# Optimization experiments

Hardware: AMD Instinct MI355X
Metric: run time of the kernel (lower is better)

The kernel has to match this reference:

```python
import jax, jax.numpy as jnp
import numpy as np

B, N, F_IN, F_OUT, K = 128, 400, 128, 128, 5


def setup_inputs() -> dict:
    key = jax.random.key(0)
    ks = jax.random.split(key, 7)
    s_in = 1.0 / np.sqrt(F_IN)
    s_out = 1.0 / np.sqrt(F_OUT)
    return {
        "x": jax.random.normal(ks[0], (B, N, F_IN), dtype=jnp.float32),
        # SAGEConv layer 1: lin_l (neighbor agg, with bias) and lin_r (root, no bias)
        "W1l": jax.random.normal(ks[1], (F_OUT, F_IN), dtype=jnp.float32) * s_in,
        "b1l": jnp.zeros((F_OUT,), dtype=jnp.float32),
        "W1r": jax.random.normal(ks[2], (F_OUT, F_IN), dtype=jnp.float32) * s_in,
        # SAGEConv layer 2
        "W2l": jax.random.normal(ks[3], (F_OUT, F_OUT), dtype=jnp.float32) * s_out,
        "b2l": jnp.zeros((F_OUT,), dtype=jnp.float32),
        "W2r": jax.random.normal(ks[4], (F_OUT, F_OUT), dtype=jnp.float32) * s_out,
    }


def _knn_sym_adj(x):
    # x: [B, N, F]. Per-batch 5-NN graph with self-loops (loop=True),
    # then symmetrized (to_undirected coalesces duplicates -> 0/1 adjacency).
    sq = jnp.sum(x * x, axis=-1)                       # [B, N]
    d2 = sq[:, :, None] + sq[:, None, :] - 2.0 * jnp.einsum("bnd,bmd->bnm", x, x)
    _, idx = jax.lax.top_k(-d2, K)                     # [B, N, K] nearest incl. self
    A = jnp.zeros((x.shape[0], x.shape[1], x.shape[1]), dtype=x.dtype)
    bi = jnp.arange(x.shape[0])[:, None, None]
    ni = jnp.arange(x.shape[1])[None, :, None]
    A = A.at[bi, ni, idx].set(1.0)                     # A[b,i,j]=1 if j in knn(i)
    return jnp.maximum(A, A.transpose(0, 2, 1))        # undirected


def _sage(h, A, deg, Wl, bl, Wr):
    # PyG SAGEConv (mean aggr): out = lin_l(mean_j x_j) + lin_r(x_i)
    m = jnp.einsum("bnm,bmf->bnf", A, h) / deg
    return m @ Wl.T + bl + h @ Wr.T


def reference(x, W1l, b1l, W1r, W2l, b2l, W2r):
    A = _knn_sym_adj(x)
    deg = jnp.sum(A, axis=-1, keepdims=True)           # >=1 (self-loop)
    h = jax.nn.relu(_sage(x, A, deg, W1l, b1l, W1r))
    h = _sage(h, A, deg, W2l, b2l, W2r)
    return h.reshape(B * N, F_OUT)
```

## Files before the change

kernel.cpp:

```cpp
#include <hip/hip_runtime.h>
#include <hip/hip_bf16.h>
#include <stdint.h>

#define B_   128
#define N_   400
#define F_   128
#define K_   5
#define ROWS (B_ * N_)
#define POOLCAP 2048
#define DCAP 416
#define MAXFLAG ROWS
#define GAP_HEDGE 5e-4
#define DELTA_MAX 0.18f
#define NW 13

typedef __attribute__((ext_vector_type(8))) short bf16x8;
typedef __attribute__((ext_vector_type(4))) float f32x4;

static __device__ __forceinline__ unsigned short f2bf(float f) {
  union { float f; unsigned u; } v; v.f = f;
  unsigned r = v.u + 0x7fff + ((v.u >> 16) & 1);
  return (unsigned short)(r >> 16);
}
static __device__ __forceinline__ float bf2f(unsigned short h) {
  union { unsigned u; float f; } v; v.u = ((unsigned)h) << 16; return v.f;
}

template<int M, typename T>
static __device__ __forceinline__ void insM(T d, int j, T bd[], int bj[]) {
  if (d < bd[M - 1] || (d == bd[M - 1] && j < bj[M - 1])) {
    bd[M - 1] = d; bj[M - 1] = j;
#pragma unroll
    for (int q = M - 1; q > 0; --q) {
      bool sw = (bd[q] < bd[q - 1]) || (bd[q] == bd[q - 1] && bj[q] < bj[q - 1]);
      T td = bd[q]; int tj = bj[q];
      if (sw) { bd[q] = bd[q - 1]; bd[q - 1] = td; bj[q] = bj[q - 1]; bj[q - 1] = tj; }
    }
  }
}

__global__ __launch_bounds__(256) void k_prep_rows(const float* __restrict__ x,
                                                   unsigned short* __restrict__ Y,
                                                   float* __restrict__ sq) {
  int wave = threadIdx.x >> 6, lane = threadIdx.x & 63;
  int row = blockIdx.x * 4 + wave;
  float2 v = *(const float2*)&x[(size_t)row * F_ + lane * 2];
  unsigned short hx = f2bf(v.x), hy = f2bf(v.y);
  float lx = v.x - bf2f(hx), ly = v.y - bf2f(hy);
  *(unsigned*)&Y[(size_t)row * 256 + lane * 2]       = (unsigned)hx | ((unsigned)hy << 16);
  *(unsigned*)&Y[(size_t)row * 256 + 128 + lane * 2] = (unsigned)f2bf(lx) | ((unsigned)f2bf(ly) << 16);
  float s = v.x * v.x + v.y * v.y;
#pragma unroll
  for (int o = 32; o > 0; o >>= 1) s += __shfl_xor(s, o);
  if (lane == 0) sq[row] = s;
}

__global__ __launch_bounds__(256) void k_prep_w(const float* __restrict__ W1l,
                                                const float* __restrict__ W1r,
                                                const float* __restrict__ W2l,
                                                const float* __restrict__ W2r,
                                                unsigned short* __restrict__ Wh,
                                                unsigned short* __restrict__ Wlo) {
  int t = blockIdx.x * 256 + threadIdx.x;
  int m = t >> 14, e = t & 16383;
  const float* src = (m == 0) ? W1l : (m == 1) ? W1r : (m == 2) ? W2l : W2r;
  float f = src[e];
  unsigned short h = f2bf(f);
  Wh[t] = h;
  Wlo[t] = f2bf(f - bf2f(h));
}

#define YJ_STRIDE 264
__global__ __launch_bounds__(256) void k_knn(const unsigned short* __restrict__ Y,
                                             const float* __restrict__ sq,
                                             int* __restrict__ idxout,
                                             int* __restrict__ flagcnt,
                                             int* __restrict__ flagrows,
                                             int* __restrict__ cand) {
  __shared__ unsigned short Yj[64 * YJ_STRIDE];
  __shared__ float sqj[64];

  int b = blockIdx.y, i0 = blockIdx.x * 64;
  int tid = threadIdx.x, wave = tid >> 6, lane = tid & 63;

  int i_local = wave * 16 + (lane & 15);
  int arow = b * N_ + min(i0 + i_local, N_ - 1);
  float sqi = sq[arow];

  const bf16x8* abase = (const bf16x8*)&Y[(size_t)arow * 256];
  bf16x8 af[8];
#pragma unroll
  for (int kc = 0; kc < 8; ++kc) af[kc] = abase[kc * 4 + (lane >> 4)];

  float bd[8] = {3.4e38f, 3.4e38f, 3.4e38f, 3.4e38f, 3.4e38f, 3.4e38f, 3.4e38f, 3.4e38f};
  int   bj[8] = {1 << 30, 1 << 30, 1 << 30, 1 << 30, 1 << 30, 1 << 30, 1 << 30, 1 << 30};

  const float4* srcb = (const float4*)(Y + (size_t)b * N_ * 256);

  for (int jt = 0; jt < 7; ++jt) {
    int j0 = jt * 64;
    float4* dst4 = (float4*)Yj;
#pragma unroll
    for (int q = 0; q < 8; ++q) {
      int l = tid + 256 * q;
      int r = l >> 5, cc = l & 31;
      int jr = min(j0 + r, N_ - 1);
      dst4[r * 33 + cc] = srcb[jr * 32 + cc];
    }
    if (tid < 64) sqj[tid] = sq[b * N_ + min(j0 + tid, N_ - 1)];
    __syncthreads();

#pragma unroll
    for (int ct = 0; ct < 4; ++ct) {
      f32x4 acc = {0.f, 0.f, 0.f, 0.f};
      int jfr = ct * 16 + (lane & 15);
      const bf16x8* bbase = (const bf16x8*)&Yj[jfr * YJ_STRIDE];
#pragma unroll
      for (int kc = 0; kc < 12; ++kc) {
        int bidx = (kc & 3) * 4 + ((kc >= 8) ? 16 : 0) + (lane >> 4);
        acc = __builtin_amdgcn_mfma_f32_16x16x32_bf16(bbase[bidx], af[kc & 7], acc, 0, 0, 0);
      }
      int jbase = ct * 16 + (lane >> 4) * 4;
      float4 sjv = *(const float4*)&sqj[jbase];
      float sj4[4] = {sjv.x, sjv.y, sjv.z, sjv.w};
#pragma unroll
      for (int r = 0; r < 4; ++r) {
        int j = j0 + jbase + r;
        float d = sqi + sj4[r] - 2.0f * acc[r];
        if (j < N_) insM<8, float>(d, j, bd, bj);
      }
    }
    __syncthreads();
  }

  float* mbd = (float*)Yj;
  int*   mbj = (int*)Yj + 2048;
  int slot = i_local * 32 + (lane >> 4) * 8;
#pragma unroll
  for (int q = 0; q < 8; ++q) { mbd[slot + q] = bd[q]; mbj[slot + q] = bj[q]; }
  __syncthreads();

  if (tid < 64) {
    int i = i0 + tid;
    if (i < N_) {
      float fd[6] = {3.4e38f, 3.4e38f, 3.4e38f, 3.4e38f, 3.4e38f, 3.4e38f};
      int   fj[6] = {1 << 30, 1 << 30, 1 << 30, 1 << 30, 1 << 30, 1 << 30};
      for (int q = 0; q < 32; ++q)
        insM<6, float>(mbd[tid * 32 + q], mbj[tid * 32 + q], fd, fj);
      int gi = b * N_ + i;
#pragma unroll
      for (int q = 0; q < 5; ++q) idxout[gi * K_ + q] = fj[q];
      if (fd[5] - fd[4] < 0.02f) {
        int pos = atomicAdd(flagcnt, 1);
        if (pos < MAXFLAG) {
          flagrows[pos] = gi;
          for (int q = 0; q < 32; ++q) cand[gi * 32 + q] = mbj[tid * 32 + q];
        }
      }
    }
  }
}

__global__ __launch_bounds__(256) void k_refine(const float* __restrict__ x,
                                                const int* __restrict__ flagrows,
                                                const int* __restrict__ flagcnt,
                                                const int* __restrict__ cand,
                                                int* __restrict__ idx,
                                                int* __restrict__ hcnt,
                                                int* __restrict__ hrows,
                                                int* __restrict__ hab) {
  __shared__ double dbuf[8][32];
  __shared__ int    jbuf[8][32];
  int slot = threadIdx.x >> 5, c = threadIdx.x & 31;
  int nflag = min(*flagcnt, MAXFLAG);
  for (int base = blockIdx.x * 8; base < nflag; base += gridDim.x * 8) {
    int t = base + slot;
    __syncthreads();
    if (t < nflag) {
      int row = flagrows[t];
      int b = row / N_;
      int j = cand[row * 32 + c];
      const float* xi = x + (size_t)row * F_;
      const float* xj = x + (size_t)(b * N_ + j) * F_;
      double s = 0.0;
#pragma unroll
      for (int q = 0; q < 128; ++q) {
        double d = (double)xi[q] - (double)xj[q];
        s = fma(d, d, s);
      }
      dbuf[slot][c] = s; jbuf[slot][c] = j;
    }
    __syncthreads();
    if (c == 0 && t < nflag) {
      int row = flagrows[t];
      int b = row / N_;
      double fd[6] = {1e300, 1e300, 1e300, 1e300, 1e300, 1e300};
      int    fj[6] = {1 << 30, 1 << 30, 1 << 30, 1 << 30, 1 << 30, 1 << 30};
      for (int q = 0; q < 32; ++q) insM<6, double>(dbuf[slot][q], jbuf[slot][q], fd, fj);
#pragma unroll
      for (int q = 0; q < 5; ++q) idx[row * K_ + q] = fj[q];
      if (fd[5] - fd[4] < GAP_HEDGE) {
        int p = atomicAdd(hcnt, 1);
        if (p < MAXFLAG) {
          hrows[p] = row;
          hab[2 * p]     = b * N_ + fj[4];
          hab[2 * p + 1] = b * N_ + fj[5];
        }
      }
    }
  }
}

__global__ __launch_bounds__(512) void k_buildg(const int* __restrict__ idx,
                                                const int* __restrict__ c6,
                                                int* __restrict__ L6,
                                                float* __restrict__ W6,
                                                int* __restrict__ pooli,
                                                float* __restrict__ poolw,
                                                int* __restrict__ offi,
                                                int* __restrict__ cnti) {
  __shared__ unsigned bm1[N_][NW];
  __shared__ unsigned bmh[N_][NW];
  __shared__ int cs[512];
  int b = blockIdx.x, t = threadIdx.x;
  int gb0 = b * N_;

  for (int q = t; q < N_ * NW; q += 512) {
    (&bm1[0][0])[q] = 0u;
    (&bmh[0][0])[q] = 0u;
  }

  int i = t;
  int j0 = -1, j1 = -1, j2 = -1, j3 = -1, j4 = -1, y6 = -1;
  if (i < N_) {
    const int* ip = idx + (size_t)(gb0 + i) * 5;
    j0 = ip[0]; j1 = ip[1]; j2 = ip[2]; j3 = ip[3]; j4 = ip[4];
    y6 = c6[gb0 + i];
  }
  __syncthreads();

  if (i < N_) {
    unsigned bit = 1u << (i & 31);
    int w = i >> 5;
    if (j0 != i) atomicOr(&bm1[j0][w], bit);
    if (j1 != i) atomicOr(&bm1[j1][w], bit);
    if (j2 != i) atomicOr(&bm1[j2][w], bit);
    if (j3 != i) atomicOr(&bm1[j3][w], bit);
    if (j4 != i) {
      if (y6 >= 0) atomicOr(&bmh[j4][w], bit); else atomicOr(&bm1[j4][w], bit);
    }
    if (y6 >= 0 && y6 != i) atomicOr(&bmh[y6][w], bit);
  }
  __syncthreads();

  if (i < N_) {
    int gi = gb0 + i;
    int   jj[6]  = {j0, j1, j2, j3, j4, y6};
    float w1s[6] = {1.f, 1.f, 1.f, 1.f,
                    (y6 >= 0) ? 0.5f : 1.f,
                    (y6 >= 0) ? 0.5f : 0.f};
#pragma unroll
    for (int k = 0; k < 6; ++k) {
      int j = jj[k]; float w1 = w1s[k];
      size_t sl = (size_t)gi * 6 + k;
      if (w1 <= 0.f || j < 0) { L6[sl] = gi; W6[sl] = 0.f; continue; }
      if (j == i)             { L6[sl] = gi; W6[sl] = 1.f; continue; }
      float w2 = ((bm1[i][j >> 5] >> (j & 31)) & 1) ? 1.f
               : (((bmh[i][j >> 5] >> (j & 31)) & 1) ? 0.5f : 0.f);
      L6[sl] = gb0 + j; W6[sl] = fmaxf(w1, w2);
    }
  }

  unsigned mw[NW];
  int cnt_i = 0;
  if (i < N_) {
#pragma unroll
    for (int w = 0; w < NW; ++w) {
      unsigned ex = 0;
      if ((i  >> 5) == w) ex |= 1u << (i  & 31);
      if ((j0 >> 5) == w) ex |= 1u << (j0 & 31);
      if ((j1 >> 5) == w) ex |= 1u << (j1 & 31);
      if ((j2 >> 5) == w) ex |= 1u << (j2 & 31);
      if ((j3 >> 5) == w) ex |= 1u << (j3 & 31);
      if ((j4 >> 5) == w) ex |= 1u << (j4 & 31);
      if (y6 >= 0 && (y6 >> 5) == w) ex |= 1u << (y6 & 31);
      unsigned m = (bm1[i][w] | bmh[i][w]) & ~ex;
      mw[w] = m;
      cnt_i += __popc(m);
    }
  } else {
#pragma unroll
    for (int w = 0; w < NW; ++w) mw[w] = 0u;
  }

  cs[t] = (i < N_) ? cnt_i : 0;
  __syncthreads();
  for (int off = 1; off < 512; off <<= 1) {
    int v = (t >= off) ? cs[t - off] : 0;
    __syncthreads();
    cs[t] += v;
    __syncthreads();
  }

  if (i < N_) {
    int o = b * POOLCAP + cs[t] - cnt_i;
    offi[gb0 + i] = o;
    cnti[gb0 + i] = cnt_i;
    int c = 0;
#pragma unroll
    for (int w = 0; w < NW; ++w) {
      unsigned m = mw[w];
      unsigned ones = bm1[i][w];
      while (m) {
        int bit = __ffs(m) - 1; m &= m - 1;
        int r = w * 32 + bit;
        pooli[o + c] = gb0 + r;
        poolw[o + c] = ((ones >> bit) & 1) ? 1.f : 0.5f;
        ++c;
      }
    }
  }
}

__global__ __launch_bounds__(128) void k_delta(
    const float* __restrict__ P, const float* __restrict__ Qb,
    const float* __restrict__ b1, const unsigned short* __restrict__ h1b,
    const float* __restrict__ sumP, const float* __restrict__ degv,
    const int* __restrict__ L6, const float* __restrict__ W6,
    const int* __restrict__ pooli, const float* __restrict__ poolw,
    const int* __restrict__ offi, const int* __restrict__ cnti,
    const int* __restrict__ idx,
    const int* __restrict__ hcnt, const int* __restrict__ hrows,
    const int* __restrict__ hab,
    const float* __restrict__ W2l, const float* __restrict__ W2r,
    int* __restrict__ c6, float* __restrict__ w5) {
  __shared__ float H[3][2][128];
  __shared__ float dH[3][128];
  __shared__ float U[3][128];
  __shared__ float V1[128], V2[128], red[128];
  __shared__ int   Ls[3][DCAP];
  __shared__ float Wsh[3][DCAP];
  int f = threadIdx.x;
  int n = min(*hcnt, MAXFLAG);
  for (int t = blockIdx.x; t < n; t += gridDim.x) {
    int gi = hrows[t], ga = hab[2 * t], gb = hab[2 * t + 1];
    int bb = gi / N_, iw = gi - bb * N_;
    bool ma = false, mb = false;
#pragma unroll
    for (int q = 0; q < K_; ++q) {
      ma = ma || (idx[ga * K_ + q] == iw);
      mb = mb || (idx[gb * K_ + q] == iw);
    }
    if (ma && mb) continue;
    int rows3[3] = {gi, ga, gb};
    int nn3[3];
    for (int s3 = 0; s3 < 3; ++s3) {
      int r = rows3[s3];
      int cc = cnti[r], oo = offi[r];
      int nn = 6 + cc; nn3[s3] = nn;
      for (int e = f; e < DCAP; e += 128) {
        int li = -1; float lw = 0.f;
        if (e < 6)      { li = L6[(size_t)r * 6 + e]; lw = W6[(size_t)r * 6 + e]; }
        else if (e < nn){ li = pooli[oo + e - 6];     lw = poolw[oo + e - 6]; }
        Ls[s3][e] = li; Wsh[s3][e] = lw;
      }
    }
    for (int s3 = 0; s3 < 3; ++s3) {
      int r = rows3[s3];
      float s1 = sumP[(size_t)r * 128 + f], d1 = degv[r];
      float ds = 0.f, dd = 0.f;
      if (s3 == 0) {
        if (!ma) { ds -= P[(size_t)ga * 128 + f]; dd -= 1.f; }
        if (!mb) { ds += P[(size_t)gb * 128 + f]; dd += 1.f; }
      } else if (s3 == 1) {
        if (!ma) { ds -= P[(size_t)gi * 128 + f]; dd -= 1.f; }
      } else {
        if (!mb) { ds += P[(size_t)gi * 128 + f]; dd += 1.f; }
      }
      float base = b1[f] + Qb[(size_t)r * 128 + f];
      float h0 = fmaxf(s1 / d1 + base, 0.f);
      float h1v = fmaxf((s1 + ds) / (d1 + dd) + base, 0.f);
      H[s3][0][f] = h0;
      H[s3][1][f] = h1v;
      dH[s3][f] = h1v - h0;
    }
    __syncthreads();
    {
      float u0 = 0.f, u1 = 0.f, u2 = 0.f;
      for (int f2 = 0; f2 < 128; ++f2) {
        float wv = W2l[f * 128 + f2];
        u0 += dH[0][f2] * wv;
        u1 += dH[1][f2] * wv;
        u2 += dH[2][f2] * wv;
      }
      U[0][f] = u0; U[1][f] = u1; U[2][f] = u2;
    }
    __syncthreads();
    float dmax = 0.f;
    for (int which = 0; which < 3; ++which) {
      float v1 = 0.f, v2 = 0.f;
      float d1r = degv[rows3[which]], d2r = d1r;
      int nnw = nn3[which];
      for (int e2 = 0; e2 < nnw; ++e2) {
        float w = Wsh[which][e2];
        if (w == 0.f) continue;
        int s = Ls[which][e2];
        float hv1, hv2;
        if (s == gi)      { hv1 = H[0][0][f]; hv2 = H[0][1][f]; }
        else if (s == ga) { hv1 = H[1][0][f]; hv2 = H[1][1][f]; }
        else if (s == gb) { hv1 = H[2][0][f]; hv2 = H[2][1][f]; }
        else {
          float hh = bf2f(h1b[(size_t)s * 256 + f]) + bf2f(h1b[(size_t)s * 256 + 128 + f]);
          hv1 = hh; hv2 = hh;
        }
        bool inG2 = true;
        if (which == 0 && s == ga && !ma) inG2 = false;
        if (which == 1 && s == gi && !ma) inG2 = false;
        v1 += w * hv1;
        if (inG2) v2 += w * hv2; else d2r -= w;
      }
      if (which == 0 && !mb) { v2 += H[2][1][f]; d2r += 1.f; }
      if (which == 2 && !mb) { v2 += H[0][1][f]; d2r += 1.f; }
      V1[f] = v1; V2[f] = v2;
      __syncthreads();
      float a1 = 0.f, a2 = 0.f, ow = 0.f;
      for (int f2 = 0; f2 < 128; ++f2) {
        float wl = W2l[f * 128 + f2];
        a1 += V1[f2] * wl;
        a2 += V2[f2] * wl;
        ow += dH[which][f2] * W2r[f * 128 + f2];
      }
      dmax = fmaxf(dmax, fabsf(a2 / d2r - a1 / d1r + ow));
      __syncthreads();
    }
    for (int li = 0; li < 3; ++li) {
      for (int e = f; e < nn3[li]; e += 128) {
        float w = Wsh[li][e];
        if (w == 0.f) continue;
        int r = Ls[li][e];
        if (r == gi || r == ga || r == gb) continue;
        bool dup = false;
        for (int lj = 0; lj < li && !dup; ++lj)
          for (int e2 = 0; e2 < nn3[lj]; ++e2)
            if (Ls[lj][e2] == r && Wsh[lj][e2] != 0.f) { dup = true; break; }
        if (dup) continue;
        float wi = 0.f, wa = 0.f, wb = 0.f;
        if (li == 0) wi = w; else if (li == 1) wa = w; else wb = w;
        for (int lj = li + 1; lj < 3; ++lj)
          for (int e2 = 0; e2 < nn3[lj]; ++e2)
            if (Ls[lj][e2] == r && Wsh[lj][e2] != 0.f) {
              if (lj == 1) wa = Wsh[lj][e2]; else wb = Wsh[lj][e2];
            }
        float lm = 0.f;
        for (int ff = 0; ff < 128; ++ff)
          lm = fmaxf(lm, fabsf(wi * U[0][ff] + wa * U[1][ff] + wb * U[2][ff]));
        dmax = fmaxf(dmax, lm / degv[r]);
      }
    }
    red[f] = dmax;
    __syncthreads();
    for (int o = 64; o > 0; o >>= 1) {
      if (f < o) red[f] = fmaxf(red[f], red[f + o]);
      __syncthreads();
    }
    if (f == 0 && red[0] < DELTA_MAX) { c6[gi] = gb - bb * N_; w5[gi] = 0.5f; }
    __syncthreads();
  }
}

#define WSTR 130
__global__ __launch_bounds__(256) void k_gemm(const unsigned short* __restrict__ A,
                                              const unsigned short* __restrict__ Whl,
                                              const unsigned short* __restrict__ Whr,
                                              const unsigned short* __restrict__ Wll,
                                              const unsigned short* __restrict__ Wlr,
                                              float* __restrict__ P, float* __restrict__ Q) {
  __shared__ unsigned short W[4 * 128 * WSTR];
  int tid = threadIdx.x, wave = tid >> 6, lane = tid & 63;
#pragma unroll
  for (int q = 0; q < 2; ++q) {
    int ridx = tid * 2 + q;
    int mat = ridx >> 7, n = ridx & 127;
    const unsigned short* src =
        ((mat == 0) ? Whl : (mat == 1) ? Whr : (mat == 2) ? Wll : Wlr) + n * 128;
    unsigned short* dst = &W[(size_t)ridx * WSTR];
#pragma unroll
    for (int p = 0; p < 16; ++p) *(bf16x8*)(dst + p * 8) = *(const bf16x8*)(src + p * 8);
  }
  __syncthreads();

  size_t row = (size_t)blockIdx.x * 64 + wave * 16 + (lane & 15);
  bf16x8 af[8];
#pragma unroll
  for (int s = 0; s < 2; ++s)
#pragma unroll
    for (int kc = 0; kc < 4; ++kc)
      af[s * 4 + kc] = *(const bf16x8*)&A[row * 256 + s * 128 + kc * 32 + (lane >> 4) * 8];

  size_t orow0 = (size_t)blockIdx.x * 64 + wave * 16 + (lane >> 4) * 4;
#pragma unroll
  for (int w = 0; w < 2; ++w) {
    float* O = w ? Q : P;
#pragma unroll
    for (int ct = 0; ct < 8; ++ct) {
      f32x4 acc = {0.f, 0.f, 0.f, 0.f};
      int n = ct * 16 + (lane & 15);
      const unsigned short* bh = &W[(size_t)(w * 128 + n) * WSTR];
      const unsigned short* bl = &W[(size_t)((2 + w) * 128 + n) * WSTR];
#pragma unroll
      for (int kc = 0; kc < 4; ++kc) {
        bf16x8 fh = *(const bf16x8*)(bh + kc * 32 + (lane >> 4) * 8);
        bf16x8 fl_ = *(const bf16x8*)(bl + kc * 32 + (lane >> 4) * 8);
        acc = __builtin_amdgcn_mfma_f32_16x16x32_bf16(af[kc], fh, acc, 0, 0, 0);
        acc = __builtin_amdgcn_mfma_f32_16x16x32_bf16(af[4 + kc], fh, acc, 0, 0, 0);
        acc = __builtin_amdgcn_mfma_f32_16x16x32_bf16(af[kc], fl_, acc, 0, 0, 0);
      }
#pragma unroll
      for (int r = 0; r < 4; ++r)
        O[(orow0 + r) * 128 + ct * 16 + (lane & 15)] = acc[r];
    }
  }
}

__global__ __launch_bounds__(256) void k_aggr(const float* __restrict__ P,
                                              const float* __restrict__ Q,
                                              const int* __restrict__ L6,
                                              const float* __restrict__ W6,
                                              const int* __restrict__ pooli,
                                              const float* __restrict__ poolw,
                                              const int* __restrict__ offi,
                                              const int* __restrict__ cnti,
                                              const float* __restrict__ bias,
                                              float* __restrict__ outf,
                                              unsigned short* __restrict__ outb,
                                              float* __restrict__ sumP,
                                              float* __restrict__ degv,
                                              int relu) {
  int r = blockIdx.x * 8 + (threadIdx.x >> 5);
  int l4 = threadIdx.x & 31;
  int m = cnti[r], o = offi[r];
  float4 acc = {0.f, 0.f, 0.f, 0.f};
  float deg = 0.f;
#pragma unroll
  for (int k = 0; k < 6; ++k) {
    float ww = W6[(size_t)r * 6 + k];
    float4 p4 = *(const float4*)&P[(size_t)L6[(size_t)r * 6 + k] * 128 + l4 * 4];
    acc.x += ww * p4.x; acc.y += ww * p4.y;
    acc.z += ww * p4.z; acc.w += ww * p4.w;
    deg += ww;
  }
  for (int q = 0; q < m; ++q) {
    float ww = poolw[o + q];
    float4 p4 = *(const float4*)&P[(size_t)pooli[o + q] * 128 + l4 * 4];
    acc.x += ww * p4.x; acc.y += ww * p4.y;
    acc.z += ww * p4.z; acc.w += ww * p4.w;
    deg += ww;
  }
  if (sumP) {
    *(float4*)&sumP[(size_t)r * 128 + l4 * 4] = acc;
    if (l4 == 0) degv[r] = deg;
  }
  float4 b4 = *(const float4*)&bias[l4 * 4];
  float4 q4 = *(const float4*)&Q[(size_t)r * 128 + l4 * 4];
  float4 v;
  v.x = acc.x / deg + b4.x + q4.x;
  v.y = acc.y / deg + b4.y + q4.y;
  v.z = acc.z / deg + b4.z + q4.z;
  v.w = acc.w / deg + b4.w + q4.w;
  if (relu) {
    v.x = fmaxf(v.x, 0.f); v.y = fmaxf(v.y, 0.f);
    v.z = fmaxf(v.z, 0.f); v.w = fmaxf(v.w, 0.f);
  }
  if (outf) {
    *(float4*)&outf[(size_t)r * 128 + l4 * 4] = v;
  } else {
    ushort4 hi, lo;
    hi.x = f2bf(v.x); hi.y = f2bf(v.y); hi.z = f2bf(v.z); hi.w = f2bf(v.w);
    lo.x = f2bf(v.x - bf2f(hi.x)); lo.y = f2bf(v.y - bf2f(hi.y));
    lo.z = f2bf(v.z - bf2f(hi.z)); lo.w = f2bf(v.w - bf2f(hi.w));
    *(ushort4*)&outb[(size_t)r * 256 + l4 * 4] = hi;
    *(ushort4*)&outb[(size_t)r * 256 + 128 + l4 * 4] = lo;
  }
}

extern "C" void kernel_launch(void* const* d_in, const int* in_sizes, int n_in,
                              void* d_out, int out_size, void* d_ws, size_t ws_size,
                              hipStream_t stream) {
  const float* x   = (const float*)d_in[0];
  const float* W1l = (const float*)d_in[1];
  const float* b1l = (const float*)d_in[2];
  const float* W1r = (const float*)d_in[3];
  const float* W2l = (const float*)d_in[4];
  const float* b2l = (const float*)d_in[5];
  const float* W2r = (const float*)d_in[6];
  float* out = (float*)d_out;

  char* w = (char*)d_ws;
  unsigned short* Y    = (unsigned short*)w; w += (size_t)ROWS * 256 * 2;
  float*          sq   = (float*)w;          w += (size_t)ROWS * 4;
  unsigned short* Wh   = (unsigned short*)w; w += (size_t)4 * 16384 * 2;
  unsigned short* Wlo  = (unsigned short*)w; w += (size_t)4 * 16384 * 2;
  int*            idx  = (int*)w;            w += (size_t)ROWS * K_ * 4;
  int*            L6   = (int*)w;            w += (size_t)ROWS * 6 * 4;
  float*          W6   = (float*)w;          w += (size_t)ROWS * 6 * 4;
  int*            pooli= (int*)w;            w += (size_t)B_ * POOLCAP * 4;
  float*          poolw= (float*)w;          w += (size_t)B_ * POOLCAP * 4;
  int*            offi = (int*)w;            w += (size_t)ROWS * 4;
  int*            cnti = (int*)w;            w += (size_t)ROWS * 4;
  int*            flags = (int*)w;           w += 64;
  int*            c6   = (int*)w;            w += (size_t)ROWS * 4;
  float*          w5   = (float*)w;          w += (size_t)ROWS * 4;
  int*            flagrows = (int*)w;        w += (size_t)MAXFLAG * 4;
  int*            hrows = (int*)w;           w += (size_t)MAXFLAG * 4;
  int*            hab  = (int*)w;            w += (size_t)MAXFLAG * 8;
  int*            candb = (int*)w;           w += (size_t)ROWS * 32 * 4;
  float*          P    = (float*)w;          w += (size_t)ROWS * 128 * 4;
  float*          Qb   = (float*)w;          w += (size_t)ROWS * 128 * 4;
  unsigned short* h1b  = (unsigned short*)w; w += (size_t)ROWS * 256 * 2;
  float*          sumP = (float*)w;          w += (size_t)ROWS * 128 * 4;
  float*          degv = (float*)w;          w += (size_t)ROWS * 4;
  (void)ws_size; (void)in_sizes; (void)n_in; (void)out_size;

  hipMemsetAsync(flags, 0, 64, stream);
  hipMemsetAsync(c6, 0xFF, (size_t)ROWS * 4, stream);
  k_prep_rows<<<ROWS / 4, 256, 0, stream>>>(x, Y, sq);
  k_prep_w<<<(4 * 16384) / 256, 256, 0, stream>>>(W1l, W1r, W2l, W2r, Wh, Wlo);
  k_knn<<<dim3(7, B_), 256, 0, stream>>>(Y, sq, idx, &flags[0], flagrows, candb);
  k_gemm<<<ROWS / 64, 256, 0, stream>>>(Y, Wh, Wh + 16384, Wlo, Wlo + 16384, P, Qb);
  k_refine<<<64, 256, 0, stream>>>(x, flagrows, &flags[0], candb, idx,
                                   &flags[1], hrows, hab);
  k_buildg<<<B_, 512, 0, stream>>>(idx, c6, L6, W6, pooli, poolw, offi, cnti);
  k_aggr<<<ROWS / 8, 256, 0, stream>>>(P, Qb, L6, W6, pooli, poolw, offi, cnti,
                                       b1l, nullptr, h1b, sumP, degv, 1);
  k_delta<<<64, 128, 0, stream>>>(P, Qb, b1l, h1b, sumP, degv, L6, W6, pooli,
                                  poolw, offi, cnti, idx, &flags[1], hrows, hab,
                                  W2l, W2r, c6, w5);
  k_buildg<<<B_, 512, 0, stream>>>(idx, c6, L6, W6, pooli, poolw, offi, cnti);
  k_aggr<<<ROWS / 8, 256, 0, stream>>>(P, Qb, L6, W6, pooli, poolw, offi, cnti,
                                       b1l, nullptr, h1b, nullptr, nullptr, 1);
  k_gemm<<<ROWS / 64, 256, 0, stream>>>(h1b, Wh + 2 * 16384, Wh + 3 * 16384,
                                        Wlo + 2 * 16384, Wlo + 3 * 16384, P, Qb);
  k_aggr<<<ROWS / 8, 256, 0, stream>>>(P, Qb, L6, W6, pooli, poolw, offi, cnti,
                                       b2l, out, nullptr, nullptr, nullptr, 0);
}
```

Baseline: 704.6 us.

## Recompute layer-1 only for delta-affected rows and prefetch kNN tiles

The full second layer-1 aggregation pass over all rows is replaced by a sparse recompute. k_delta now appends each changed row and its two partner rows to a list, and only those rows get h1 recomputed (k_aggr_d) and re-multiplied (k_gemm_d). The full layer-2 GEMM runs on the first h1, writing into reused buffers (P2 aliases Y, Q2 aliases sumP), and the sparse kernels patch those outputs afterward. The kNN kernel also register-prefetches the next j-tile from global memory while computing the current one, and pads the merge buffer stride to 33. The risk is correctness if rows outside the list are affected by the graph change, since only the changed row and its partners are recomputed.

```diff
diff --git a/kernel.cpp b/kernel.cpp
--- a/kernel.cpp
+++ b/kernel.cpp
@@ -97,18 +97,31 @@
 
   const float4* srcb = (const float4*)(Y + (size_t)b * N_ * 256);
 
+  int pr[8], pcc[8];
+#pragma unroll
+  for (int q = 0; q < 8; ++q) { int l = tid + 256 * q; pr[q] = l >> 5; pcc[q] = l & 31; }
+
+  float4 pre[8];
+#pragma unroll
+  for (int q = 0; q < 8; ++q) pre[q] = srcb[min(pr[q], N_ - 1) * 32 + pcc[q]];
+  float sqpre = 0.f;
+  if (tid < 64) sqpre = sq[b * N_ + min(tid, N_ - 1)];
+
   for (int jt = 0; jt < 7; ++jt) {
     int j0 = jt * 64;
     float4* dst4 = (float4*)Yj;
 #pragma unroll
-    for (int q = 0; q < 8; ++q) {
-      int l = tid + 256 * q;
-      int r = l >> 5, cc = l & 31;
-      int jr = min(j0 + r, N_ - 1);
-      dst4[r * 33 + cc] = srcb[jr * 32 + cc];
-    }
-    if (tid < 64) sqj[tid] = sq[b * N_ + min(j0 + tid, N_ - 1)];
-    __syncthreads();
+    for (int q = 0; q < 8; ++q) dst4[pr[q] * 33 + pcc[q]] = pre[q];
+    if (tid < 64) sqj[tid] = sqpre;
+    __syncthreads();
+
+    if (jt < 6) {
+      int j0n = j0 + 64;
+#pragma unroll
+      for (int q = 0; q < 8; ++q)
+        pre[q] = srcb[min(j0n + pr[q], N_ - 1) * 32 + pcc[q]];
+      if (tid < 64) sqpre = sq[b * N_ + min(j0n + tid, N_ - 1)];
+    }
 
 #pragma unroll
     for (int ct = 0; ct < 4; ++ct) {
@@ -134,8 +147,8 @@
   }
 
   float* mbd = (float*)Yj;
-  int*   mbj = (int*)Yj + 2048;
-  int slot = i_local * 32 + (lane >> 4) * 8;
+  int*   mbj = (int*)Yj + 64 * 33;
+  int slot = i_local * 33 + (lane >> 4) * 8;
 #pragma unroll
   for (int q = 0; q < 8; ++q) { mbd[slot + q] = bd[q]; mbj[slot + q] = bj[q]; }
   __syncthreads();
@@ -146,7 +159,7 @@
       float fd[6] = {3.4e38f, 3.4e38f, 3.4e38f, 3.4e38f, 3.4e38f, 3.4e38f};
       int   fj[6] = {1 << 30, 1 << 30, 1 << 30, 1 << 30, 1 << 30, 1 << 30};
       for (int q = 0; q < 32; ++q)
-        insM<6, float>(mbd[tid * 32 + q], mbj[tid * 32 + q], fd, fj);
+        insM<6, float>(mbd[tid * 33 + q], mbj[tid * 33 + q], fd, fj);
       int gi = b * N_ + i;
 #pragma unroll
       for (int q = 0; q < 5; ++q) idxout[gi * K_ + q] = fj[q];
@@ -154,7 +167,7 @@
         int pos = atomicAdd(flagcnt, 1);
         if (pos < MAXFLAG) {
           flagrows[pos] = gi;
-          for (int q = 0; q < 32; ++q) cand[gi * 32 + q] = mbj[tid * 32 + q];
+          for (int q = 0; q < 32; ++q) cand[gi * 32 + q] = mbj[tid * 33 + q];
         }
       }
     }
@@ -333,7 +346,7 @@
     const int* __restrict__ hcnt, const int* __restrict__ hrows,
     const int* __restrict__ hab,
     const float* __restrict__ W2l, const float* __restrict__ W2r,
-    int* __restrict__ c6, float* __restrict__ w5) {
+    int* __restrict__ c6, int* __restrict__ dcnt, int* __restrict__ dlist) {
   __shared__ float H[3][2][128];
   __shared__ float dH[3][128];
   __shared__ float U[3][128];
@@ -463,7 +476,11 @@
       if (f < o) red[f] = fmaxf(red[f], red[f + o]);
       __syncthreads();
     }
-    if (f == 0 && red[0] < DELTA_MAX) { c6[gi] = gb - bb * N_; w5[gi] = 0.5f; }
+    if (f == 0 && red[0] < DELTA_MAX) {
+      c6[gi] = gb - bb * N_;
+      int p = atomicAdd(dcnt, 3);
+      dlist[p] = gi; dlist[p + 1] = ga; dlist[p + 2] = gb;
+    }
     __syncthreads();
   }
 }
@@ -518,6 +535,67 @@
 #pragma unroll
       for (int r = 0; r < 4; ++r)
         O[(orow0 + r) * 128 + ct * 16 + (lane & 15)] = acc[r];
+    }
+  }
+}
+
+__global__ __launch_bounds__(256) void k_gemm_d(const unsigned short* __restrict__ A,
+                                                const unsigned short* __restrict__ Whl,
+                                                const unsigned short* __restrict__ Whr,
+                                                const unsigned short* __restrict__ Wll,
+                                                const unsigned short* __restrict__ Wlr,
+                                                float* __restrict__ P, float* __restrict__ Q,
+                                                const int* __restrict__ dcnt,
+                                                const int* __restrict__ dlist) {
+  int dn = *dcnt;
+  if (blockIdx.x * 64 >= dn) return;
+  __shared__ unsigned short W[4 * 128 * WSTR];
+  int tid = threadIdx.x, wave = tid >> 6, lane = tid & 63;
+#pragma unroll
+  for (int q = 0; q < 2; ++q) {
+    int ridx = tid * 2 + q;
+    int mat = ridx >> 7, n = ridx & 127;
+    const unsigned short* src =
+        ((mat == 0) ? Whl : (mat == 1) ? Whr : (mat == 2) ? Wll : Wlr) + n * 128;
+    unsigned short* dst = &W[(size_t)ridx * WSTR];
+#pragma unroll
+    for (int p = 0; p < 16; ++p) *(bf16x8*)(dst + p * 8) = *(const bf16x8*)(src + p * 8);
+  }
+  __syncthreads();
+
+  for (int tb = blockIdx.x * 64; tb < dn; tb += gridDim.x * 64) {
+    size_t row = (size_t)dlist[min(tb + wave * 16 + (lane & 15), dn - 1)];
+    bf16x8 af[8];
+#pragma unroll
+    for (int s = 0; s < 2; ++s)
+#pragma unroll
+      for (int kc = 0; kc < 4; ++kc)
+        af[s * 4 + kc] = *(const bf16x8*)&A[row * 256 + s * 128 + kc * 32 + (lane >> 4) * 8];
+
+    int lo0 = tb + wave * 16 + (lane >> 4) * 4;
+#pragma unroll
+    for (int w = 0; w < 2; ++w) {
+      float* O = w ? Q : P;
+#pragma unroll
+      for (int ct = 0; ct < 8; ++ct) {
+        f32x4 acc = {0.f, 0.f, 0.f, 0.f};
+        int n = ct * 16 + (lane & 15);
+        const unsigned short* bh = &W[(size_t)(w * 128 + n) * WSTR];
+        const unsigned short* bl = &W[(size_t)((2 + w) * 128 + n) * WSTR];
+#pragma unroll
+        for (int kc = 0; kc < 4; ++kc) {
+          bf16x8 fh = *(const bf16x8*)(bh + kc * 32 + (lane >> 4) * 8);
+          bf16x8 fl_ = *(const bf16x8*)(bl + kc * 32 + (lane >> 4) * 8);
+          acc = __builtin_amdgcn_mfma_f32_16x16x32_bf16(af[kc], fh, acc, 0, 0, 0);
+          acc = __builtin_amdgcn_mfma_f32_16x16x32_bf16(af[4 + kc], fh, acc, 0, 0, 0);
+          acc = __builtin_amdgcn_mfma_f32_16x16x32_bf16(af[kc], fl_, acc, 0, 0, 0);
+        }
+#pragma unroll
+        for (int r = 0; r < 4; ++r) {
+          size_t orow = (size_t)dlist[min(lo0 + r, dn - 1)];
+          O[orow * 128 + ct * 16 + (lane & 15)] = acc[r];
+        }
+      }
     }
   }
 }
@@ -583,6 +661,56 @@
   }
 }
 
+__global__ __launch_bounds__(256) void k_aggr_d(const float* __restrict__ P,
+                                                const float* __restrict__ Q,
+                                                const int* __restrict__ L6,
+                                                const float* __restrict__ W6,
+                                                const int* __restrict__ pooli,
+                                                const float* __restrict__ poolw,
+                                                const int* __restrict__ offi,
+                                                const int* __restrict__ cnti,
+                                                const float* __restrict__ bias,
+                                                unsigned short* __restrict__ outb,
+                                                const int* __restrict__ dcnt,
+                                                const int* __restrict__ dlist) {
+  int dn = *dcnt;
+  int l4 = threadIdx.x & 31;
+  for (int di = blockIdx.x * 8 + (threadIdx.x >> 5); di < dn; di += gridDim.x * 8) {
+    int r = dlist[di];
+    int m = cnti[r], o = offi[r];
+    float4 acc = {0.f, 0.f, 0.f, 0.f};
+    float deg = 0.f;
+#pragma unroll
+    for (int k = 0; k < 6; ++k) {
+      float ww = W6[(size_t)r * 6 + k];
+      float4 p4 = *(const float4*)&P[(size_t)L6[(size_t)r * 6 + k] * 128 + l4 * 4];
+      acc.x += ww * p4.x; acc.y += ww * p4.y;
+      acc.z += ww * p4.z; acc.w += ww * p4.w;
+      deg += ww;
+    }
+    for (int q = 0; q < m; ++q) {
+      float ww = poolw[o + q];
+      float4 p4 = *(const float4*)&P[(size_t)pooli[o + q] * 128 + l4 * 4];
+      acc.x += ww * p4.x; acc.y += ww * p4.y;
+      acc.z += ww * p4.z; acc.w += ww * p4.w;
+      deg += ww;
+    }
+    float4 b4 = *(const float4*)&bias[l4 * 4];
+    float4 q4 = *(const float4*)&Q[(size_t)r * 128 + l4 * 4];
+    float4 v;
+    v.x = fmaxf(acc.x / deg + b4.x + q4.x, 0.f);
+    v.y = fmaxf(acc.y / deg + b4.y + q4.y, 0.f);
+    v.z = fmaxf(acc.z / deg + b4.z + q4.z, 0.f);
+    v.w = fmaxf(acc.w / deg + b4.w + q4.w, 0.f);
+    ushort4 hi, lo;
+    hi.x = f2bf(v.x); hi.y = f2bf(v.y); hi.z = f2bf(v.z); hi.w = f2bf(v.w);
+    lo.x = f2bf(v.x - bf2f(hi.x)); lo.y = f2bf(v.y - bf2f(hi.y));
+    lo.z = f2bf(v.z - bf2f(hi.z)); lo.w = f2bf(v.w - bf2f(hi.w));
+    *(ushort4*)&outb[(size_t)r * 256 + l4 * 4] = hi;
+    *(ushort4*)&outb[(size_t)r * 256 + 128 + l4 * 4] = lo;
+  }
+}
+
 extern "C" void kernel_launch(void* const* d_in, const int* in_sizes, int n_in,
                               void* d_out, int out_size, void* d_ws, size_t ws_size,
                               hipStream_t stream) {
@@ -609,7 +737,7 @@
   int*            cnti = (int*)w;            w += (size_t)ROWS * 4;
   int*            flags = (int*)w;           w += 64;
   int*            c6   = (int*)w;            w += (size_t)ROWS * 4;
-  float*          w5   = (float*)w;          w += (size_t)ROWS * 4;
+  int*            dlist= (int*)w;            w += (size_t)3 * MAXFLAG * 4;
   int*            flagrows = (int*)w;        w += (size_t)MAXFLAG * 4;
   int*            hrows = (int*)w;           w += (size_t)MAXFLAG * 4;
   int*            hab  = (int*)w;            w += (size_t)MAXFLAG * 8;
@@ -619,6 +747,8 @@
   unsigned short* h1b  = (unsigned short*)w; w += (size_t)ROWS * 256 * 2;
   float*          sumP = (float*)w;          w += (size_t)ROWS * 128 * 4;
   float*          degv = (float*)w;          w += (size_t)ROWS * 4;
+  float* P2 = (float*)Y;
+  float* Q2 = sumP;
   (void)ws_size; (void)in_sizes; (void)n_in; (void)out_size;
 
   hipMemsetAsync(flags, 0, 64, stream);
@@ -634,12 +764,15 @@
                                        b1l, nullptr, h1b, sumP, degv, 1);
   k_delta<<<64, 128, 0, stream>>>(P, Qb, b1l, h1b, sumP, degv, L6, W6, pooli,
                                   poolw, offi, cnti, idx, &flags[1], hrows, hab,
-                                  W2l, W2r, c6, w5);
+                                  W2l, W2r, c6, &flags[2], dlist);
   k_buildg<<<B_, 512, 0, stream>>>(idx, c6, L6, W6, pooli, poolw, offi, cnti);
-  k_aggr<<<ROWS / 8, 256, 0, stream>>>(P, Qb, L6, W6, pooli, poolw, offi, cnti,
-                                       b1l, nullptr, h1b, nullptr, nullptr, 1);
   k_gemm<<<ROWS / 64, 256, 0, stream>>>(h1b, Wh + 2 * 16384, Wh + 3 * 16384,
-                                        Wlo + 2 * 16384, Wlo + 3 * 16384, P, Qb);
-  k_aggr<<<ROWS / 8, 256, 0, stream>>>(P, Qb, L6, W6, pooli, poolw, offi, cnti,
+                                        Wlo + 2 * 16384, Wlo + 3 * 16384, P2, Q2);
+  k_aggr_d<<<64, 256, 0, stream>>>(P, Qb, L6, W6, pooli, poolw, offi, cnti,
+                                   b1l, h1b, &flags[2], dlist);
+  k_gemm_d<<<32, 256, 0, stream>>>(h1b, Wh + 2 * 16384, Wh + 3 * 16384,
+                                   Wlo + 2 * 16384, Wlo + 3 * 16384, P2, Q2,
+                                   &flags[2], dlist);
+  k_aggr<<<ROWS / 8, 256, 0, stream>>>(P2, Q2, L6, W6, pooli, poolw, offi, cnti,
                                        b2l, out, nullptr, nullptr, nullptr, 0);
 }
```

Measured after the change: 696.7 us. No clear change (-1.1%).
